# Kernel tuning notes

Measured on AMD Instinct MI355X. Metric: run time of the kernel, lower is better.

The kernel has to match this reference:

```python
import jax, jax.numpy as jnp
import numpy as np

B, S, D = 4, 2048, 2048
H, HD = 16, 128
ROPE_THETA = 10000.0


def rotate_half(x):
    half = x.shape[-1] // 2
    return jnp.concatenate([-x[..., half:], x[..., :half]], axis=-1)


def setup_inputs() -> dict:
    key = jax.random.key(0)
    ks = jax.random.split(key, 5)
    scale = 1.0 / np.sqrt(D)
    x = jax.random.normal(ks[0], (B, S, D), dtype=jnp.float32)
    wq = jax.random.normal(ks[1], (D, H * HD), dtype=jnp.float32) * scale
    wk = jax.random.normal(ks[2], (D, H * HD), dtype=jnp.float32) * scale
    wv = jax.random.normal(ks[3], (D, H * HD), dtype=jnp.float32) * scale
    wo = jax.random.normal(ks[4], (H * HD, D), dtype=jnp.float32) * scale
    # RoPE frequencies: freqs_cis real/imag parts, shape [S, HD//2]
    inv_freq = 1.0 / (ROPE_THETA ** (np.arange(0, HD, 2, dtype=np.float32) / HD))
    t = np.arange(S, dtype=np.float32)
    freqs = np.outer(t, inv_freq)  # [S, HD//2]
    cos = jnp.asarray(np.cos(freqs), dtype=jnp.float32)
    sin = jnp.asarray(np.sin(freqs), dtype=jnp.float32)
    return {"x": x, "wq": wq, "wk": wk, "wv": wv, "wo": wo, "cos": cos, "sin": sin}


def reference(x, wq, wk, wv, wo, cos, sin):
    batch, seq_len, _ = x.shape
    # QKV projections (no bias), reshape to [b, h, s, d]
    q = (x @ wq).reshape(batch, seq_len, H, HD).transpose(0, 2, 1, 3)
    k = (x @ wk).reshape(batch, seq_len, H, HD).transpose(0, 2, 1, 3)
    v = (x @ wv).reshape(batch, seq_len, H, HD)  # [b, s, h, d]
    # RoPE (half-split / rotate_half convention)
    cos_full = jnp.concatenate([cos, cos], axis=-1)[None, None, :seq_len, :]
    sin_full = jnp.concatenate([sin, sin], axis=-1)[None, None, :seq_len, :]
    q = q * cos_full + rotate_half(q) * sin_full
    k = k * cos_full + rotate_half(k) * sin_full
    # Scaled dot-product attention with causal mask
    logits = jnp.einsum('bhqd,bhkd->bhqk', q, k) / jnp.sqrt(jnp.float32(HD))
    causal = jnp.tril(jnp.ones((seq_len, seq_len), dtype=bool))
    logits = jnp.where(causal[None, None, :, :], logits, -1e10)
    weights = jax.nn.softmax(logits, axis=-1)
    out = jnp.einsum('bhqk,bkhd->bqhd', weights, v)
    out = out.reshape(batch, seq_len, H * HD)
    return out @ wo
```

## Files before the change

### kernel.cpp

```cpp
#include <hip/hip_runtime.h>
#include <cstdint>
#include <cstddef>

typedef unsigned short u16;
using bf16x8  = __attribute__((ext_vector_type(8))) short;
using floatx4 = __attribute__((ext_vector_type(4))) float;

__device__ __forceinline__ u16 f2bf(float f) {
    union { float f; unsigned u; } v; v.f = f;
    unsigned r = v.u + 0x7fffu + ((v.u >> 16) & 1u);
    return (u16)(r >> 16);
}
__device__ __forceinline__ float bf2f(u16 h) {
    union { unsigned u; float f; } v; v.u = ((unsigned)h) << 16; return v.f;
}
__device__ __forceinline__ floatx4 mfma16(bf16x8 a, bf16x8 b, floatx4 c) {
    return __builtin_amdgcn_mfma_f32_16x16x32_bf16(a, b, c, 0, 0, 0);
}
using gptr_t = const __attribute__((address_space(1))) unsigned int*;
using lptr_t = __attribute__((address_space(3))) unsigned int*;
__device__ __forceinline__ void lds16(const void* g, void* l) {
    __builtin_amdgcn_global_load_lds((gptr_t)g, (lptr_t)l, 16, 0, 0);
}

#define ATT_SCALE 0.1275758218522532f

__global__ __launch_bounds__(256) void cvt_x(const float* __restrict__ x, u16* __restrict__ xb) {
    size_t i = ((size_t)blockIdx.x * 256 + threadIdx.x) * 4;
    float4 v = *(const float4*)&x[i];
    ushort4 r; r.x = f2bf(v.x); r.y = f2bf(v.y); r.z = f2bf(v.z); r.w = f2bf(v.w);
    *(ushort4*)&xb[i] = r;
}

__global__ __launch_bounds__(256) void transpose_wall(const float* __restrict__ wq, const float* __restrict__ wk,
                                                      const float* __restrict__ wv, const float* __restrict__ wo,
                                                      u16* __restrict__ wqkvb, u16* __restrict__ wob) {
    __shared__ float t[64][65];
    const int z = blockIdx.z;
    const float* in = (z == 0) ? wq : (z == 1) ? wk : (z == 2) ? wv : wo;
    u16* out = (z < 3) ? (wqkvb + (size_t)z * 2048 * 2048) : wob;
    int k0 = blockIdx.x * 64, n0 = blockIdx.y * 64;
    int tx = threadIdx.x, ty = threadIdx.y;
#pragma unroll
    for (int i = 0; i < 16; ++i) {
        int r = i * 4 + ty;
        t[r][tx] = in[(size_t)(k0 + r) * 2048 + n0 + tx];
    }
    __syncthreads();
#pragma unroll
    for (int i = 0; i < 16; ++i) {
        int r = i * 4 + ty;
        out[(size_t)(n0 + r) * 2048 + k0 + tx] = f2bf(t[tx][r]);
    }
}

template <int MODE>
__global__ __launch_bounds__(256, 5) void gemm_bt(const u16* __restrict__ A, const u16* __restrict__ B,
                                                  u16* __restrict__ Qo, u16* __restrict__ Ko, u16* __restrict__ Vt,
                                                  float* __restrict__ Co) {
    __shared__ __align__(16) u16 As[128 * 64];
    __shared__ __align__(16) u16 Bs[128 * 64];
    const int m0 = blockIdx.y << 7;
    const int n0 = blockIdx.x << 7;
    const int tid = threadIdx.x;
    const int w = tid >> 6, lane = tid & 63;
    const int wm = w >> 1, wn = w & 1;
    const int m16 = lane & 15, q4 = lane >> 4;

    floatx4 acc[4][4];
#pragma unroll
    for (int r = 0; r < 4; ++r)
#pragma unroll
        for (int c = 0; c < 4; ++c) acc[r][c] = (floatx4)0.0f;

    const u16* Abase = A + (size_t)(m0 + w * 32 + (lane >> 3)) * 2048 + (lane & 7) * 8;
    const u16* Bbase = B + (size_t)(n0 + w * 32 + (lane >> 3)) * 2048 + (lane & 7) * 8;
    u16* lA = As + (w * 32) * 64;
    u16* lB = Bs + (w * 32) * 64;

    for (int kt = 0; kt < 32; ++kt) {
        __syncthreads();
        const u16* ga = Abase + kt * 64;
        const u16* gb = Bbase + kt * 64;
#pragma unroll
        for (int t = 0; t < 4; ++t) {
            lds16(ga + (size_t)t * 8 * 2048, lA + t * 8 * 64);
            lds16(gb + (size_t)t * 8 * 2048, lB + t * 8 * 64);
        }
        __syncthreads();
#pragma unroll
        for (int kk = 0; kk < 2; ++kk) {
            bf16x8 af[4], bfr[4];
#pragma unroll
            for (int r = 0; r < 4; ++r)
                af[r] = *(const bf16x8*)&As[(wm * 64 + r * 16 + m16) * 64 + kk * 32 + q4 * 8];
#pragma unroll
            for (int c = 0; c < 4; ++c)
                bfr[c] = *(const bf16x8*)&Bs[(wn * 64 + c * 16 + m16) * 64 + kk * 32 + q4 * 8];
#pragma unroll
            for (int r = 0; r < 4; ++r)
#pragma unroll
                for (int c = 0; c < 4; ++c)
                    acc[r][c] = mfma16(af[r], bfr[c], acc[r][c]);
        }
    }

    if (MODE == 0) {
        const int which = n0 >> 11;
        const int h = (n0 >> 7) & 15;
        if (which < 2) {
            u16* dst = (which == 0) ? Qo : Ko;
#pragma unroll
            for (int r = 0; r < 4; ++r) {
#pragma unroll
                for (int c = 0; c < 4; ++c) {
                    int d = wn * 64 + c * 16 + m16;
                    int mbase = m0 + wm * 64 + r * 16 + q4 * 4;
#pragma unroll
                    for (int i = 0; i < 4; ++i) {
                        int mm = mbase + i;
                        int b = mm >> 11, s = mm & 2047;
                        dst[((size_t)((b * 16 + h) * 2048 + s) << 7) + d] = f2bf(acc[r][c][i]);
                    }
                }
            }
        } else {
#pragma unroll
            for (int r = 0; r < 4; ++r) {
#pragma unroll
                for (int c = 0; c < 4; ++c) {
                    int d = wn * 64 + c * 16 + m16;
                    int mbase = m0 + wm * 64 + r * 16 + q4 * 4;
                    int b = mbase >> 11, s = mbase & 2047;
                    ushort4 pk;
                    pk.x = f2bf(acc[r][c][0]); pk.y = f2bf(acc[r][c][1]);
                    pk.z = f2bf(acc[r][c][2]); pk.w = f2bf(acc[r][c][3]);
                    *(ushort4*)&Vt[((size_t)((b * 16 + h) * 128 + d)) * 2048 + s] = pk;
                }
            }
        }
    } else {
#pragma unroll
        for (int r = 0; r < 4; ++r) {
#pragma unroll
            for (int c = 0; c < 4; ++c) {
                int n = n0 + wn * 64 + c * 16 + m16;
                int mbase = m0 + wm * 64 + r * 16 + q4 * 4;
#pragma unroll
                for (int i = 0; i < 4; ++i)
                    Co[(size_t)(mbase + i) * 2048 + n] = acc[r][c][i];
            }
        }
    }
}

__global__ __launch_bounds__(256) void rope_qk(u16* __restrict__ Q, u16* __restrict__ K,
                                               const float* __restrict__ cosb, const float* __restrict__ sinb) {
    int t = blockIdx.x * 256 + threadIdx.x;
    int d4 = (t & 15) * 4;
    int row = t >> 4;
    int s = row & 2047;
    float4 cs = *(const float4*)&cosb[s * 64 + d4];
    float4 sn = *(const float4*)&sinb[s * 64 + d4];
    size_t base = (size_t)row * 128;
    ushort4 qlo = *(ushort4*)&Q[base + d4];
    ushort4 qhi = *(ushort4*)&Q[base + 64 + d4];
    ushort4 klo = *(ushort4*)&K[base + d4];
    ushort4 khi = *(ushort4*)&K[base + 64 + d4];
    float ql[4] = {bf2f(qlo.x), bf2f(qlo.y), bf2f(qlo.z), bf2f(qlo.w)};
    float qh[4] = {bf2f(qhi.x), bf2f(qhi.y), bf2f(qhi.z), bf2f(qhi.w)};
    float kl[4] = {bf2f(klo.x), bf2f(klo.y), bf2f(klo.z), bf2f(klo.w)};
    float kh[4] = {bf2f(khi.x), bf2f(khi.y), bf2f(khi.z), bf2f(khi.w)};
    float c[4] = {cs.x, cs.y, cs.z, cs.w};
    float n[4] = {sn.x, sn.y, sn.z, sn.w};
    ushort4 o0, o1, o2, o3;
    u16* p0 = &o0.x; u16* p1 = &o1.x; u16* p2 = &o2.x; u16* p3 = &o3.x;
#pragma unroll
    for (int i = 0; i < 4; ++i) {
        p0[i] = f2bf((ql[i] * c[i] - qh[i] * n[i]) * ATT_SCALE);
        p1[i] = f2bf((qh[i] * c[i] + ql[i] * n[i]) * ATT_SCALE);
        p2[i] = f2bf(kl[i] * c[i] - kh[i] * n[i]);
        p3[i] = f2bf(kh[i] * c[i] + kl[i] * n[i]);
    }
    *(ushort4*)&Q[base + d4]      = o0;
    *(ushort4*)&Q[base + 64 + d4] = o1;
    *(ushort4*)&K[base + d4]      = o2;
    *(ushort4*)&K[base + 64 + d4] = o3;
}

__global__ __launch_bounds__(512) void attn_kernel(const u16* __restrict__ Q, const u16* __restrict__ K,
                                                   const u16* __restrict__ VT, u16* __restrict__ AO) {
    __shared__ __align__(16) u16 ks[64 * 136];
    __shared__ __align__(16) u16 vts[128 * 72];
    __shared__ __align__(16) u16 ps[256 * 72];
    static const int iqmap[8] = {7, 6, 5, 4, 0, 1, 2, 3};
    const int bx = blockIdx.x;
    const int iq = iqmap[bx >> 6];
    const int bh = bx & 63;
    const int b = bh >> 4, h = bh & 15;
    const u16* Qg = Q  + (size_t)bh * (2048 * 128);
    const u16* Kg = K  + (size_t)bh * (2048 * 128);
    const u16* Vg = VT + (size_t)bh * (128 * 2048);
    const int tid = threadIdx.x, w = tid >> 6, lane = tid & 63;
    const int m16 = lane & 15, q4 = lane >> 4;
    const int jn = 4 * iq + 4;

    const int qrow = iq * 256 + w * 32;
    bf16x8 qf[2][4];
#pragma unroll
    for (int rm = 0; rm < 2; ++rm)
#pragma unroll
        for (int kk = 0; kk < 4; ++kk)
            qf[rm][kk] = *(const bf16x8*)&Qg[(size_t)(qrow + rm * 16 + m16) * 128 + kk * 32 + q4 * 8];

    floatx4 o[2][8];
#pragma unroll
    for (int rm = 0; rm < 2; ++rm)
#pragma unroll
        for (int c = 0; c < 8; ++c) o[rm][c] = (floatx4)0.0f;
    float mrow[2] = {-1e30f, -1e30f}, lrow[2] = {0.0f, 0.0f};

    for (int j = 0; j < jn; ++j) {
        __syncthreads();
#pragma unroll
        for (int u = 0; u < 2; ++u) {
            int id = u * 512 + tid;
            int kr = id >> 4, kc = id & 15;
            uint4 kv = *(const uint4*)&Kg[(size_t)(j * 64 + kr) * 128 + kc * 8];
            int vr = id >> 3, vc = id & 7;
            uint4 vv = *(const uint4*)&Vg[(size_t)vr * 2048 + j * 64 + vc * 8];
            *(uint4*)&ks[kr * 136 + kc * 8] = kv;
            *(uint4*)&vts[vr * 72 + vc * 8] = vv;
        }
        __syncthreads();

        floatx4 sacc[2][4];
#pragma unroll
        for (int rm = 0; rm < 2; ++rm)
#pragma unroll
            for (int r = 0; r < 4; ++r) sacc[rm][r] = (floatx4)0.0f;
#pragma unroll
        for (int kk = 0; kk < 4; ++kk) {
            bf16x8 kb[4];
#pragma unroll
            for (int r = 0; r < 4; ++r)
                kb[r] = *(const bf16x8*)&ks[(r * 16 + m16) * 136 + kk * 32 + q4 * 8];
#pragma unroll
            for (int rm = 0; rm < 2; ++rm)
#pragma unroll
                for (int r = 0; r < 4; ++r)
                    sacc[rm][r] = mfma16(kb[r], qf[rm][kk], sacc[rm][r]);
        }

        if (j >= 4 * iq) {
#pragma unroll
            for (int rm = 0; rm < 2; ++rm) {
                const int qg = qrow + rm * 16 + m16;
#pragma unroll
                for (int r = 0; r < 4; ++r)
#pragma unroll
                    for (int i = 0; i < 4; ++i) {
                        int kg = j * 64 + r * 16 + q4 * 4 + i;
                        if (kg > qg) sacc[rm][r][i] = -1e30f;
                    }
            }
        }

#pragma unroll
        for (int rm = 0; rm < 2; ++rm) {
            float pmax = -1e30f;
#pragma unroll
            for (int r = 0; r < 4; ++r)
#pragma unroll
                for (int i = 0; i < 4; ++i) pmax = fmaxf(pmax, sacc[rm][r][i]);
            pmax = fmaxf(pmax, __shfl_xor(pmax, 16));
            pmax = fmaxf(pmax, __shfl_xor(pmax, 32));
            float mnew = fmaxf(mrow[rm], pmax);
            float alpha = __builtin_amdgcn_exp2f(mrow[rm] - mnew);
            mrow[rm] = mnew;

            float psum = 0.0f;
#pragma unroll
            for (int r = 0; r < 4; ++r) {
                float p0 = __builtin_amdgcn_exp2f(sacc[rm][r][0] - mnew);
                float p1 = __builtin_amdgcn_exp2f(sacc[rm][r][1] - mnew);
                float p2 = __builtin_amdgcn_exp2f(sacc[rm][r][2] - mnew);
                float p3 = __builtin_amdgcn_exp2f(sacc[rm][r][3] - mnew);
                psum += (p0 + p1) + (p2 + p3);
                ushort4 pk; pk.x = f2bf(p0); pk.y = f2bf(p1); pk.z = f2bf(p2); pk.w = f2bf(p3);
                *(ushort4*)&ps[(w * 32 + rm * 16 + m16) * 72 + r * 16 + q4 * 4] = pk;
            }
            psum += __shfl_xor(psum, 16);
            psum += __shfl_xor(psum, 32);
            lrow[rm] = lrow[rm] * alpha + psum;

            float abc[4];
#pragma unroll
            for (int i = 0; i < 4; ++i) abc[i] = __shfl(alpha, q4 * 4 + i);
#pragma unroll
            for (int c = 0; c < 8; ++c)
#pragma unroll
                for (int i = 0; i < 4; ++i) o[rm][c][i] *= abc[i];
        }

#pragma unroll
        for (int kk = 0; kk < 2; ++kk) {
            bf16x8 pa[2];
#pragma unroll
            for (int rm = 0; rm < 2; ++rm)
                pa[rm] = *(const bf16x8*)&ps[(w * 32 + rm * 16 + m16) * 72 + kk * 32 + q4 * 8];
#pragma unroll
            for (int ch = 0; ch < 2; ++ch) {
                bf16x8 vb[4];
#pragma unroll
                for (int c = 0; c < 4; ++c)
                    vb[c] = *(const bf16x8*)&vts[((ch * 4 + c) * 16 + m16) * 72 + kk * 32 + q4 * 8];
#pragma unroll
                for (int rm = 0; rm < 2; ++rm)
#pragma unroll
                    for (int c = 0; c < 4; ++c)
                        o[rm][ch * 4 + c] = mfma16(pa[rm], vb[c], o[rm][ch * 4 + c]);
            }
        }
    }

#pragma unroll
    for (int rm = 0; rm < 2; ++rm) {
        float linv = __builtin_amdgcn_rcpf(lrow[rm]);
        float li[4];
#pragma unroll
        for (int i = 0; i < 4; ++i) li[i] = __shfl(linv, q4 * 4 + i);
#pragma unroll
        for (int c = 0; c < 8; ++c)
#pragma unroll
            for (int i = 0; i < 4; ++i) {
                int s = qrow + rm * 16 + q4 * 4 + i;
                int d = c * 16 + m16;
                AO[((size_t)(b * 2048 + s)) * 2048 + h * 128 + d] = f2bf(o[rm][c][i] * li[i]);
            }
    }
}

extern "C" void kernel_launch(void* const* d_in, const int* in_sizes, int n_in,
                              void* d_out, int out_size, void* d_ws, size_t ws_size,
                              hipStream_t stream) {
    const float* x    = (const float*)d_in[0];
    const float* wq   = (const float*)d_in[1];
    const float* wk   = (const float*)d_in[2];
    const float* wv   = (const float*)d_in[3];
    const float* wo   = (const float*)d_in[4];
    const float* cosb = (const float*)d_in[5];
    const float* sinb = (const float*)d_in[6];
    float* out = (float*)d_out;

    char* ws = (char*)d_ws;
    u16* xb    = (u16*)(ws);
    u16* AO    = xb;
    u16* wqkvb = (u16*)(ws + 33554432);
    u16* wob   = (u16*)(ws + 58720256);
    u16* Qb    = (u16*)(ws + 67108864);
    u16* Kb    = (u16*)(ws + 100663296);
    u16* Vtb   = (u16*)(ws + 134217728);

    cvt_x<<<16384, 256, 0, stream>>>(x, xb);
    transpose_wall<<<dim3(32, 32, 4), dim3(64, 4), 0, stream>>>(wq, wk, wv, wo, wqkvb, wob);

    gemm_bt<0><<<dim3(48, 64), 256, 0, stream>>>(xb, wqkvb, Qb, Kb, Vtb, nullptr);
    rope_qk<<<8192, 256, 0, stream>>>(Qb, Kb, cosb, sinb);
    attn_kernel<<<512, 512, 0, stream>>>(Qb, Kb, Vtb, AO);
    gemm_bt<1><<<dim3(16, 64), 256, 0, stream>>>(AO, wob, nullptr, nullptr, nullptr, out);
}
```

Measured before the change: 616.2 us.

## Rewrite projection GEMM as 256x256 double-buffered pipelined tile with swizzled LDS

Rewrites the bf16 projection GEMM to use 256x256 output tiles per 512-thread block. Global-to-LDS loads are double-buffered and interleaved with four MFMA quadrants under fine-grained barriers and s_setprio. LDS is XOR-swizzled to avoid bank conflicts, and block IDs are remapped across 8 groups so neighbouring tiles share inputs in cache. The aim is more data reuse and loads hidden behind compute. The cost is higher register and LDS use (64KB), which lowers occupancy, and fewer blocks in the output projection (256), which may underfill the GPU.

```diff
diff --git a/kernel.cpp b/kernel.cpp
--- a/kernel.cpp
+++ b/kernel.cpp
@@ -55,100 +55,150 @@
 }
 
 template <int MODE>
-__global__ __launch_bounds__(256, 5) void gemm_bt(const u16* __restrict__ A, const u16* __restrict__ B,
+__global__ __launch_bounds__(512, 2) void gemm_bt(const u16* __restrict__ A, const u16* __restrict__ B,
                                                   u16* __restrict__ Qo, u16* __restrict__ Ko, u16* __restrict__ Vt,
                                                   float* __restrict__ Co) {
-    __shared__ __align__(16) u16 As[128 * 64];
-    __shared__ __align__(16) u16 Bs[128 * 64];
-    const int m0 = blockIdx.y << 7;
-    const int n0 = blockIdx.x << 7;
+    __shared__ __align__(16) u16 sA[2][16384];
+    __shared__ __align__(16) u16 sB[2][16384];
+
+    const int nbx = (MODE == 0) ? 24 : 8;
+    const int bid = blockIdx.x;
+    const int q8 = (int)gridDim.x >> 3;
+    const int wg = (bid & 7) * q8 + (bid >> 3);
+    const int bx = wg % nbx, by = wg / nbx;
+    const int m0 = by << 8, n0 = bx << 8;
+
     const int tid = threadIdx.x;
     const int w = tid >> 6, lane = tid & 63;
-    const int wm = w >> 1, wn = w & 1;
+    const int wm = w >> 2, wn = w & 3;
     const int m16 = lane & 15, q4 = lane >> 4;
-
-    floatx4 acc[4][4];
-#pragma unroll
-    for (int r = 0; r < 4; ++r)
+    const int lr = lane >> 3;
+    const int lc8 = (lane & 7) ^ lr;
+
+    const u16* Ag = A + (size_t)(m0 + w * 16 + lr) * 2048 + lc8 * 8;
+    const u16* Bg = B + (size_t)(n0 + w * 16 + lr) * 2048 + lc8 * 8;
+
+    const int swz0 = ((q4 ^ (m16 & 7)) << 3);
+    const int swz1 = (((4 + q4) ^ (m16 & 7)) << 3);
+
+    floatx4 acc[8][4];
+#pragma unroll
+    for (int r = 0; r < 8; ++r)
 #pragma unroll
         for (int c = 0; c < 4; ++c) acc[r][c] = (floatx4)0.0f;
-
-    const u16* Abase = A + (size_t)(m0 + w * 32 + (lane >> 3)) * 2048 + (lane & 7) * 8;
-    const u16* Bbase = B + (size_t)(n0 + w * 32 + (lane >> 3)) * 2048 + (lane & 7) * 8;
-    u16* lA = As + (w * 32) * 64;
-    u16* lB = Bs + (w * 32) * 64;
-
-    for (int kt = 0; kt < 32; ++kt) {
-        __syncthreads();
-        const u16* ga = Abase + kt * 64;
-        const u16* gb = Bbase + kt * 64;
-#pragma unroll
-        for (int t = 0; t < 4; ++t) {
-            lds16(ga + (size_t)t * 8 * 2048, lA + t * 8 * 64);
-            lds16(gb + (size_t)t * 8 * 2048, lB + t * 8 * 64);
-        }
-        __syncthreads();
-#pragma unroll
-        for (int kk = 0; kk < 2; ++kk) {
-            bf16x8 af[4], bfr[4];
-#pragma unroll
-            for (int r = 0; r < 4; ++r)
-                af[r] = *(const bf16x8*)&As[(wm * 64 + r * 16 + m16) * 64 + kk * 32 + q4 * 8];
-#pragma unroll
-            for (int c = 0; c < 4; ++c)
-                bfr[c] = *(const bf16x8*)&Bs[(wn * 64 + c * 16 + m16) * 64 + kk * 32 + q4 * 8];
-#pragma unroll
-            for (int r = 0; r < 4; ++r)
-#pragma unroll
-                for (int c = 0; c < 4; ++c)
-                    acc[r][c] = mfma16(af[r], bfr[c], acc[r][c]);
-        }
-    }
+    bf16x8 af[4][2];
+    bf16x8 bf[4][2];
+
+#define STAGE_A(b, h, t) do { \
+    lds16(Ag + (size_t)((h) * 128) * 2048 + (t) * 64,     &sA[b][(h) * 8192 + w * 1024]);       \
+    lds16(Ag + (size_t)((h) * 128 + 8) * 2048 + (t) * 64, &sA[b][(h) * 8192 + w * 1024 + 512]); \
+} while (0)
+#define STAGE_B(b, h, t) do { \
+    lds16(Bg + (size_t)((h) * 128) * 2048 + (t) * 64,     &sB[b][(h) * 8192 + w * 1024]);       \
+    lds16(Bg + (size_t)((h) * 128 + 8) * 2048 + (t) * 64, &sB[b][(h) * 8192 + w * 1024 + 512]); \
+} while (0)
+#define BAR() do { asm volatile("" ::: "memory"); __builtin_amdgcn_s_barrier(); asm volatile("" ::: "memory"); } while (0)
+#define LDA_(cur, mq) do { _Pragma("unroll") for (int fr = 0; fr < 4; ++fr) { \
+    const u16* p = &sA[cur][(wm * 128 + (mq) * 64 + fr * 16 + m16) * 64];      \
+    af[fr][0] = *(const bf16x8*)&p[swz0];                                      \
+    af[fr][1] = *(const bf16x8*)&p[swz1]; } } while (0)
+#define LDB_(cur, nq) do { _Pragma("unroll") for (int c = 0; c < 2; ++c) {     \
+    const u16* p = &sB[cur][(wn * 64 + ((nq) * 2 + c) * 16 + m16) * 64];       \
+    bf[(nq) * 2 + c][0] = *(const bf16x8*)&p[swz0];                            \
+    bf[(nq) * 2 + c][1] = *(const bf16x8*)&p[swz1]; } } while (0)
+#define MM_(mq, nq) do { _Pragma("unroll") for (int kk = 0; kk < 2; ++kk)      \
+    _Pragma("unroll") for (int fr = 0; fr < 4; ++fr)                           \
+    _Pragma("unroll") for (int c = 0; c < 2; ++c)                              \
+        acc[(mq) * 4 + fr][(nq) * 2 + c] =                                     \
+            mfma16(af[fr][kk], bf[(nq) * 2 + c][kk], acc[(mq) * 4 + fr][(nq) * 2 + c]); } while (0)
+
+    const int NT = 32;
+
+    STAGE_B(0, 0, 0); STAGE_B(0, 1, 0);
+    STAGE_A(0, 0, 0); STAGE_A(0, 1, 0);
+    STAGE_B(1, 0, 1); STAGE_B(1, 1, 1);
+    asm volatile("s_waitcnt vmcnt(4)" ::: "memory");
+    __builtin_amdgcn_s_barrier();
+
+#pragma unroll 2
+    for (int t = 0; t < NT; ++t) {
+        const int cur = t & 1;
+        LDB_(cur, 0);
+        LDA_(cur, 0);
+        if (t + 1 < NT) STAGE_A(cur ^ 1, 0, t + 1);
+        BAR();
+        __builtin_amdgcn_s_setprio(1); MM_(0, 0); __builtin_amdgcn_s_setprio(0);
+        BAR();
+        LDB_(cur, 1);
+        if (t + 1 < NT) STAGE_A(cur ^ 1, 1, t + 1);
+        BAR();
+        __builtin_amdgcn_s_setprio(1); MM_(0, 1); __builtin_amdgcn_s_setprio(0);
+        BAR();
+        LDA_(cur, 1);
+        if (t + 2 < NT) STAGE_B(cur, 0, t + 2);
+        BAR();
+        __builtin_amdgcn_s_setprio(1); MM_(1, 1); __builtin_amdgcn_s_setprio(0);
+        BAR();
+        if (t + 2 < NT) STAGE_B(cur, 1, t + 2);
+        BAR();
+        __builtin_amdgcn_s_setprio(1); MM_(1, 0); __builtin_amdgcn_s_setprio(0);
+        if (t + 2 < NT)      { asm volatile("s_waitcnt vmcnt(4)" ::: "memory"); }
+        else if (t + 1 < NT) { asm volatile("s_waitcnt vmcnt(0)" ::: "memory"); }
+        BAR();
+    }
+
+#undef STAGE_A
+#undef STAGE_B
+#undef BAR
+#undef LDA_
+#undef LDB_
+#undef MM_
 
     if (MODE == 0) {
         const int which = n0 >> 11;
-        const int h = (n0 >> 7) & 15;
         if (which < 2) {
             u16* dst = (which == 0) ? Qo : Ko;
 #pragma unroll
-            for (int r = 0; r < 4; ++r) {
+            for (int fr = 0; fr < 8; ++fr) {
+                const int mb = m0 + wm * 128 + fr * 16 + q4 * 4;
 #pragma unroll
                 for (int c = 0; c < 4; ++c) {
-                    int d = wn * 64 + c * 16 + m16;
-                    int mbase = m0 + wm * 64 + r * 16 + q4 * 4;
+                    const int n = n0 + wn * 64 + c * 16 + m16;
+                    const int h = (n >> 7) & 15, d = n & 127;
 #pragma unroll
                     for (int i = 0; i < 4; ++i) {
-                        int mm = mbase + i;
-                        int b = mm >> 11, s = mm & 2047;
-                        dst[((size_t)((b * 16 + h) * 2048 + s) << 7) + d] = f2bf(acc[r][c][i]);
+                        const int mm = mb + i;
+                        const int b = mm >> 11, s = mm & 2047;
+                        dst[((size_t)((b * 16 + h) * 2048 + s) << 7) + d] = f2bf(acc[fr][c][i]);
                     }
                 }
             }
         } else {
 #pragma unroll
-            for (int r = 0; r < 4; ++r) {
+            for (int fr = 0; fr < 8; ++fr) {
+                const int mb = m0 + wm * 128 + fr * 16 + q4 * 4;
+                const int b = mb >> 11, s = mb & 2047;
 #pragma unroll
                 for (int c = 0; c < 4; ++c) {
-                    int d = wn * 64 + c * 16 + m16;
-                    int mbase = m0 + wm * 64 + r * 16 + q4 * 4;
-                    int b = mbase >> 11, s = mbase & 2047;
+                    const int n = n0 + wn * 64 + c * 16 + m16;
+                    const int h = (n >> 7) & 15, d = n & 127;
                     ushort4 pk;
-                    pk.x = f2bf(acc[r][c][0]); pk.y = f2bf(acc[r][c][1]);
-                    pk.z = f2bf(acc[r][c][2]); pk.w = f2bf(acc[r][c][3]);
+                    pk.x = f2bf(acc[fr][c][0]); pk.y = f2bf(acc[fr][c][1]);
+                    pk.z = f2bf(acc[fr][c][2]); pk.w = f2bf(acc[fr][c][3]);
                     *(ushort4*)&Vt[((size_t)((b * 16 + h) * 128 + d)) * 2048 + s] = pk;
                 }
             }
         }
     } else {
 #pragma unroll
-        for (int r = 0; r < 4; ++r) {
+        for (int fr = 0; fr < 8; ++fr) {
+            const int mb = m0 + wm * 128 + fr * 16 + q4 * 4;
 #pragma unroll
             for (int c = 0; c < 4; ++c) {
-                int n = n0 + wn * 64 + c * 16 + m16;
-                int mbase = m0 + wm * 64 + r * 16 + q4 * 4;
+                const int n = n0 + wn * 64 + c * 16 + m16;
 #pragma unroll
                 for (int i = 0; i < 4; ++i)
-                    Co[(size_t)(mbase + i) * 2048 + n] = acc[r][c][i];
+                    Co[(size_t)(mb + i) * 2048 + n] = acc[fr][c][i];
             }
         }
     }
@@ -365,8 +415,8 @@
     cvt_x<<<16384, 256, 0, stream>>>(x, xb);
     transpose_wall<<<dim3(32, 32, 4), dim3(64, 4), 0, stream>>>(wq, wk, wv, wo, wqkvb, wob);
 
-    gemm_bt<0><<<dim3(48, 64), 256, 0, stream>>>(xb, wqkvb, Qb, Kb, Vtb, nullptr);
+    gemm_bt<0><<<768, 512, 0, stream>>>(xb, wqkvb, Qb, Kb, Vtb, nullptr);
     rope_qk<<<8192, 256, 0, stream>>>(Qb, Kb, cosb, sinb);
     attn_kernel<<<512, 512, 0, stream>>>(Qb, Kb, Vtb, AO);
-    gemm_bt<1><<<dim3(16, 64), 256, 0, stream>>>(AO, wob, nullptr, nullptr, nullptr, out);
-}
+    gemm_bt<1><<<256, 512, 0, stream>>>(AO, wob, nullptr, nullptr, nullptr, out);
+}
```

New measurement: 590.2 us. 1.04x faster.
